# Kernel optimization log

Hardware: AMD Instinct MI355X
Metric: run time of the kernel (lower is better)

## Reference

```python
import jax, jax.numpy as jnp
import numpy as np

N_UP, N_DOWN, M, D, K, F, L, B = 16, 16, 4, 128, 64, 32, 3, 1024
N = N_UP + N_DOWN
H_W = 45  # round(sqrt(F*K)), hidden dim of the 2-layer w MLP
LOG2 = float(np.log(2.0))


def ssp(x):
    # shifted softplus activation used by deepqmc
    return jax.nn.softplus(x) - LOG2


def _pair_blocks(n_up, n_down):
    # replicate idx_perm(N,2) grouped by i, then idx_pair_spin partition
    n = n_up + n_down
    i = np.repeat(np.arange(n), n - 1)
    j = np.concatenate([np.concatenate([np.arange(k), np.arange(k + 1, n)]) for k in range(n)])
    blocks = []
    for mi, mj, ri, rj in [(True, True, n_up, max(n_up - 1, 0)),
                           (True, False, n_up, n_down),
                           (False, True, n_down, n_up),
                           (False, False, n_down, max(n_down - 1, 0))]:
        mask = ((i < n_up) == mi) & ((j < n_up) == mj)
        blocks.append((i[mask].reshape(ri, rj), j[mask].reshape(ri, rj)))
    return blocks

_BLOCKS = _pair_blocks(N_UP, N_DOWN)
_CHANS = [0, 1, 1, 0]  # same, anti, anti, same (w/g channel index; 2 = nuclear)


def setup_inputs() -> dict:
    key = jax.random.key(0)
    ks = jax.random.split(key, 12)
    s = 0.1
    return {
        'edges_elec': jax.random.normal(ks[0], (B, N, N, F), jnp.float32),
        'edges_nuc': jax.random.normal(ks[1], (B, N, M, F), jnp.float32),
        'X': jax.random.normal(ks[2], (1, D), jnp.float32) * s,
        'Y': jax.random.normal(ks[3], (M, K), jnp.float32) * s,
        'wW1': jax.random.normal(ks[4], (L, 3, H_W, F), jnp.float32) * s,
        'wb1': jax.random.normal(ks[5], (L, 3, H_W), jnp.float32) * s,
        'wW2': jax.random.normal(ks[6], (L, 3, K, H_W), jnp.float32) * s,
        'wb2': jax.random.normal(ks[7], (L, 3, K), jnp.float32) * s,
        'hW': jax.random.normal(ks[8], (L, K, D), jnp.float32) * s,
        'hb': jax.random.normal(ks[9], (L, K), jnp.float32) * s,
        'gW': jax.random.normal(ks[10], (L, 3, D, K), jnp.float32) * s,
        'gb': jax.random.normal(ks[11], (L, 3, D), jnp.float32) * s,
    }


def reference(edges_elec, edges_nuc, X, Y, wW1, wb1, wW2, wb2, hW, hb, gW, gb):
    def w_mlp(l, c, e):
        # 2-layer log-dim MLP: F -> H_W -> K with SSP in between
        return ssp(e @ wW1[l, c].T + wb1[l, c]) @ wW2[l, c].T + wb2[l, c]

    b = edges_nuc.shape[0]
    x = jnp.broadcast_to(X, (b, N, D))  # initial electron embeddings (n_up==n_down)
    for l in range(L):
        h = x @ hW[l].T + hb[l]  # shared h subnet: [b,N,K]
        zs = []
        for (ii, jj), c in zip(_BLOCKS, _CHANS):
            e = edges_elec[:, ii, jj, :]               # [b, ri, rj, F] gather
            msg = w_mlp(l, c, e) * h[:, jj, :]          # [b, ri, rj, K]
            zs.append(msg.sum(axis=-2))                 # segment-sum over j
        z_same = jnp.concatenate([zs[0], zs[3]], axis=-2)  # up then down
        z_anti = jnp.concatenate([zs[1], zs[2]], axis=-2)
        z_nuc = jnp.einsum('bnmk,mk->bnk', w_mlp(l, 2, edges_nuc), Y)
        update = (z_same @ gW[l, 0].T + gb[l, 0]
                  + z_anti @ gW[l, 1].T + gb[l, 1]
                  + z_nuc @ gW[l, 2].T + gb[l, 2])
        x = x + update  # resnet
    return x
```

## Files before the change

kernel.cpp:

```cpp
#include <hip/hip_runtime.h>
#include <math.h>

#define N_   32
#define NUP_ 16
#define M_   4
#define D_   128
#define K_   64
#define F_   32
#define H_   45
#define L_   3
#define LOG2_ 0.69314718055994530942f

typedef __attribute__((ext_vector_type(8))) short short8;
typedef __attribute__((ext_vector_type(4))) float float4v;

__device__ __forceinline__ float ssp(float v) {
    return __logf(fmaf(0.5f, __expf(v), 0.5f));
}

__device__ __forceinline__ unsigned short f2bf(float x) {
    unsigned int u = __float_as_uint(x);
    return (unsigned short)((u + 0x7FFFu + ((u >> 16) & 1u)) >> 16);
}

__device__ __forceinline__ unsigned int cvtpk(float x, float y) {
    unsigned int r;
    asm("v_cvt_pk_bf16_f32 %0, %1, %2" : "=v"(r) : "v"(x), "v"(y));
    return r;
}

__global__ __launch_bounds__(256) void prep_kernel(
    const float* __restrict__ wW1, const float* __restrict__ wb2_unused,
    const float* __restrict__ wW2, const float* __restrict__ wb2,
    const float* __restrict__ gW,  const float* __restrict__ hW,
    const float* __restrict__ gb,
    short* __restrict__ w1B, short* __restrict__ w2B,
    short* __restrict__ gB,  short* __restrict__ hB, float* __restrict__ gbs)
{
    int blk = blockIdx.x;
    int t = threadIdx.x;
    if (blk < 27) {
        int lc = blk / 3, nt = blk % 3;
        short* dst = w1B + (size_t)blk * 512;
        for (int idx = t; idx < 512; idx += 256) {
            int lane = idx >> 3, jj = idx & 7;
            int k = ((lane >> 4) << 3) + jj;
            int n = nt * 16 + (lane & 15);
            float v = (n < H_) ? wW1[((size_t)lc * H_ + n) * F_ + k] : 0.0f;
            dst[idx] = (short)f2bf(v);
        }
    } else if (blk < 99) {
        int b3 = blk - 27;
        int lc = b3 >> 3, rem = b3 & 7, ks = rem >> 2, nt = rem & 3;
        short* dst = w2B + (size_t)b3 * 512;
        for (int idx = t; idx < 512; idx += 256) {
            int lane = idx >> 3, jj = idx & 7;
            int p = ks * 32 + ((lane >> 4) << 3) + jj;
            int n = nt * 16 + (lane & 15);
            float v;
            if (p == 3) v = wb2[(size_t)lc * K_ + n];
            else if ((p & 3) < 3) {
                int u = (p & 3) * 16 + (p >> 2);
                v = (u < H_) ? wW2[((size_t)lc * K_ + n) * H_ + u] : 0.0f;
            } else v = 0.0f;
            dst[idx] = (short)f2bf(v);
        }
    } else if (blk < 243) {
        int g = blk - 99;
        int l = g / 48, rem = g % 48;
        short* dst = gB + (size_t)g * 512;
        for (int idx = t; idx < 512; idx += 256) {
            int lane = idx >> 3, jj = idx & 7;
            int k = (rem >> 3) * 32 + ((lane >> 4) << 3) + jj;
            int c = k >> 6, kk = k & 63;
            int n = ((rem & 7) * 16) + (lane & 15);
            dst[idx] = (short)f2bf(gW[(((size_t)l * 3 + c) * D_ + n) * K_ + kk]);
        }
    } else if (blk < 275) {
        int hh = blk - 243;
        int li = hh >> 4, rem = hh & 15;
        short* dst = hB + (size_t)hh * 512;
        for (int idx = t; idx < 512; idx += 256) {
            int lane = idx >> 3, jj = idx & 7;
            int p = (rem >> 2) * 32 + ((lane >> 4) << 3) + jj;
            int d = (p & 7) * 16 + (p >> 3);
            int n = ((rem & 3) * 16) + (lane & 15);
            dst[idx] = (short)f2bf(hW[(((size_t)(li + 1)) * K_ + n) * D_ + d]);
        }
    } else {
        for (int idx = t; idx < 384; idx += 256) {
            int l = idx >> 7, d = idx & 127;
            gbs[idx] = gb[((size_t)l * 3 + 0) * D_ + d]
                     + gb[((size_t)l * 3 + 1) * D_ + d]
                     + gb[((size_t)l * 3 + 2) * D_ + d];
        }
    }
}

__global__ __launch_bounds__(64) void h0_kernel(
    const float* __restrict__ X, const float* __restrict__ hW,
    const float* __restrict__ hb, float* __restrict__ h0)
{
    int k = threadIdx.x;
    float a = hb[k];
    const float* w = hW + (size_t)k * D_;
    #pragma unroll 8
    for (int dd = 0; dd < D_; ++dd) a += w[dd] * X[dd];
    h0[k] = a;
}

#define WSTRIDE 68
#define HDS 72
__global__ __launch_bounds__(256, 8) void edge_kernel(
    const float* __restrict__ ee, const float* __restrict__ en,
    const float* __restrict__ Y,
    const short* __restrict__ w1B, const float* __restrict__ wb1,
    const short* __restrict__ w2B,
    const float* __restrict__ h, const float* __restrict__ h0,
    unsigned short* __restrict__ zb, int l, int hmode)
{
    __shared__ float wrow[36 * WSTRIDE];
    __shared__ short hd_s[4][16 * HDS];

    const int tid  = threadIdx.x;
    const int wv   = tid >> 6;
    const int lane = tid & 63;
    const int quad = lane >> 4;
    const int l16  = lane & 15;
    const int b    = blockIdx.x >> 3;
    const int i    = ((blockIdx.x & 7) << 2) + wv;
    const int bi   = (b << 5) + i;

    {
        int row = tid >> 3;
        int col = (tid & 7) * 8;
        const float* src = hmode ? (h + ((size_t)(b * N_ + row)) * K_ + col) : (h0 + col);
        float4 v0 = *(const float4*)(src);
        float4 v1 = *(const float4*)(src + 4);
        *(float4*)(wrow + row * WSTRIDE + col)     = v0;
        *(float4*)(wrow + row * WSTRIDE + col + 4) = v1;
        if (tid < 32) {
            int r2 = tid >> 3, o2 = (tid & 7) * 8;
            float4 y0 = *(const float4*)(Y + (size_t)r2 * K_ + o2);
            float4 y1 = *(const float4*)(Y + (size_t)r2 * K_ + o2 + 4);
            *(float4*)(wrow + (32 + r2) * WSTRIDE + o2)     = y0;
            *(float4*)(wrow + (32 + r2) * WSTRIDE + o2 + 4) = y1;
        }
    }
    __syncthreads();

    const int cA = (i < NUP_) ? 0 : 1;
    short* hd = hd_s[wv];
    const float c3  = (l16 == 0) ? 1.0f : 0.0f;
    const int   ri  = i & 3;
    const int   tqi = (i & 15) >> 2;
    const int   tti = i >> 4;

    #pragma unroll
    for (int t = 0; t < 3; ++t) {
        const int c  = (t == 2) ? 2 : ((t == 0) ? cA : 1 - cA);
        const int lc = l * 3 + c;

        float4 fa = {0.f, 0.f, 0.f, 0.f}, fb = {0.f, 0.f, 0.f, 0.f};
        if (t < 2) {
            const float* ep = ee + (((size_t)bi * N_) + t * 16 + l16) * F_ + quad * 8;
            fa = *(const float4*)(ep);
            fb = *(const float4*)(ep + 4);
        } else if (l16 < M_) {
            const float* np = en + (((size_t)bi * M_) + l16) * F_ + quad * 8;
            fa = *(const float4*)(np);
            fb = *(const float4*)(np + 4);
        }
        union { short8 s; unsigned int u[4]; } A;
        A.u[0] = cvtpk(fa.x, fa.y); A.u[1] = cvtpk(fa.z, fa.w);
        A.u[2] = cvtpk(fb.x, fb.y); A.u[3] = cvtpk(fb.z, fb.w);

        float4v acc1[3];
        #pragma unroll
        for (int nt = 0; nt < 3; ++nt) {
            int col = nt * 16 + l16;
            float b1c = (col < H_) ? wb1[(size_t)lc * H_ + col] : 0.0f;
            acc1[nt] = (float4v){b1c, b1c, b1c, b1c};
            short8 bf = *(const short8*)(w1B + (((size_t)lc * 3 + nt) << 9) + (lane << 3));
            acc1[nt] = __builtin_amdgcn_mfma_f32_16x16x32_bf16(A.s, bf, acc1[nt], 0, 0, 0);
        }

        const bool deadq = (t < 2) ? ((tti == t) && (quad == tqi)) : (quad != 0);
        #pragma unroll
        for (int r = 0; r < 4; ++r) {
            float s0 = ssp(acc1[0][r]);
            float s1 = ssp(acc1[1][r]);
            float s2 = ssp(acc1[2][r]);
            uint2 pr;
            pr.x = cvtpk(s0, s1);
            pr.y = cvtpk(s2, c3);
            const bool dead = deadq && ((t == 2) || (r == ri));
            if (dead) { pr.x = 0u; pr.y = 0u; }
            *(uint2*)(hd + (quad * 4 + r) * HDS + 4 * l16) = pr;
        }

        float4v acc2[4];
        #pragma unroll
        for (int nt = 0; nt < 4; ++nt) acc2[nt] = (float4v){0.f, 0.f, 0.f, 0.f};
        #pragma unroll
        for (int ks = 0; ks < 2; ++ks) {
            short8 a2 = *(const short8*)(hd + l16 * HDS + ks * 32 + quad * 8);
            #pragma unroll
            for (int nt = 0; nt < 4; ++nt) {
                short8 bf = *(const short8*)(w2B + ((((size_t)lc * 2 + ks) * 4 + nt) << 9) + (lane << 3));
                acc2[nt] = __builtin_amdgcn_mfma_f32_16x16x32_bf16(a2, bf, acc2[nt], 0, 0, 0);
            }
        }

        float p0 = 0.f, p1 = 0.f, p2 = 0.f, p3 = 0.f;
        #pragma unroll
        for (int r = 0; r < 4; ++r) {
            const int jrow = (t == 2) ? (32 + r) : (t * 16 + quad * 4 + r);
            const float* wr = wrow + jrow * WSTRIDE + l16;
            p0 += acc2[0][r] * wr[0];
            p1 += acc2[1][r] * wr[16];
            p2 += acc2[2][r] * wr[32];
            p3 += acc2[3][r] * wr[48];
        }

        const bool qlo = (quad & 1) != 0;
        const bool qhi = (quad & 2) != 0;
        float u  = qlo ? p1 : p0;
        float us = qlo ? p0 : p1;
        u += __shfl_xor(u * 0.0f + us, 16);
        float w  = qlo ? p3 : p2;
        float ws = qlo ? p2 : p3;
        w += __shfl_xor(ws, 16);
        float v  = qhi ? w : u;
        float vs = qhi ? u : w;
        v += __shfl_xor(vs, 32);

        unsigned int pk = cvtpk(v, v);
        zb[(size_t)bi * 192 + c * 64 + lane] = (unsigned short)pk;
    }
}

#define HXS 136
__global__ __launch_bounds__(256) void fuse_kernel(
    const unsigned short* __restrict__ zb, const short* __restrict__ gB,
    const float* __restrict__ gbs, const float* __restrict__ X,
    const short* __restrict__ hB, const float* __restrict__ hb,
    float* __restrict__ xout, float* __restrict__ hout,
    int l, int first, int compute_h)
{
    __shared__ short hx_s[4][16 * HXS];

    const int tid  = threadIdx.x;
    const int wv   = tid >> 6;
    const int lane = tid & 63;
    const int quad = lane >> 4;
    const int l16  = lane & 15;
    const int bi0  = (blockIdx.x * 4 + wv) * 16;

    float4v ax[8];
    #pragma unroll
    for (int nt = 0; nt < 8; ++nt) ax[nt] = (float4v){0.f, 0.f, 0.f, 0.f};
    const short* gb_ = gB + (size_t)l * 48 * 512;
    const short* zrow = (const short*)zb + ((size_t)(bi0 + l16)) * 192;
    #pragma unroll
    for (int ks = 0; ks < 6; ++ks) {
        short8 az = *(const short8*)(zrow + ks * 32 + quad * 8);
        #pragma unroll
        for (int nt = 0; nt < 8; ++nt) {
            short8 bf = *(const short8*)(gb_ + (((size_t)ks * 8 + nt) << 9) + (lane << 3));
            ax[nt] = __builtin_amdgcn_mfma_f32_16x16x32_bf16(az, bf, ax[nt], 0, 0, 0);
        }
    }

    float gv[8], xb[8];
    #pragma unroll
    for (int nt = 0; nt < 8; ++nt) {
        gv[nt] = gbs[(size_t)l * D_ + nt * 16 + l16];
        if (first) xb[nt] = X[nt * 16 + l16];
    }
    short* hx = hx_s[wv];
    #pragma unroll
    for (int r = 0; r < 4; ++r) {
        int row = quad * 4 + r;
        size_t gi = ((size_t)(bi0 + row)) * D_ + l16;
        float xv[8];
        #pragma unroll
        for (int nt = 0; nt < 8; ++nt) {
            float xo = (first ? xb[nt] : xout[gi + nt * 16]) + gv[nt] + ax[nt][r];
            xout[gi + nt * 16] = xo;
            xv[nt] = xo;
        }
        if (compute_h) {
            union { short8 s; unsigned int u[4]; } P;
            P.u[0] = cvtpk(xv[0], xv[1]); P.u[1] = cvtpk(xv[2], xv[3]);
            P.u[2] = cvtpk(xv[4], xv[5]); P.u[3] = cvtpk(xv[6], xv[7]);
            *(short8*)(hx + row * HXS + 8 * l16) = P.s;
        }
    }
    if (!compute_h) return;

    float4v ah[4];
    #pragma unroll
    for (int nt = 0; nt < 4; ++nt) ah[nt] = (float4v){0.f, 0.f, 0.f, 0.f};
    const short* hb_ = hB + (size_t)l * 16 * 512;
    #pragma unroll
    for (int ks = 0; ks < 4; ++ks) {
        short8 a = *(const short8*)(hx + l16 * HXS + ks * 32 + quad * 8);
        #pragma unroll
        for (int nt = 0; nt < 4; ++nt) {
            short8 bf = *(const short8*)(hb_ + (((size_t)ks * 4 + nt) << 9) + (lane << 3));
            ah[nt] = __builtin_amdgcn_mfma_f32_16x16x32_bf16(a, bf, ah[nt], 0, 0, 0);
        }
    }
    float hbv[4];
    #pragma unroll
    for (int nt = 0; nt < 4; ++nt) hbv[nt] = hb[((size_t)(l + 1)) * K_ + nt * 16 + l16];
    #pragma unroll
    for (int nt = 0; nt < 4; ++nt)
        #pragma unroll
        for (int r = 0; r < 4; ++r)
            hout[((size_t)(bi0 + quad * 4 + r)) * K_ + nt * 16 + l16] = ah[nt][r] + hbv[nt];
}

extern "C" void kernel_launch(void* const* d_in, const int* in_sizes, int n_in,
                              void* d_out, int out_size, void* d_ws, size_t ws_size,
                              hipStream_t stream)
{
    const float* ee  = (const float*)d_in[0];
    const float* en  = (const float*)d_in[1];
    const float* X   = (const float*)d_in[2];
    const float* Y   = (const float*)d_in[3];
    const float* wW1 = (const float*)d_in[4];
    const float* wb1 = (const float*)d_in[5];
    const float* wW2 = (const float*)d_in[6];
    const float* wb2 = (const float*)d_in[7];
    const float* hW  = (const float*)d_in[8];
    const float* hb  = (const float*)d_in[9];
    const float* gW  = (const float*)d_in[10];
    const float* gb  = (const float*)d_in[11];
    float* xout = (float*)d_out;

    char* ws = (char*)d_ws;
    float*          h   = (float*)(ws);
    unsigned short* zb  = (unsigned short*)(ws + 8388608);
    float*          h0  = (float*)(ws + 8388608 + 12582912);
    short*          w1B = (short*)(ws + 20971520 + 256);
    short*          w2B = w1B + (size_t)27 * 512;
    short*          gB  = w2B + (size_t)72 * 512;
    short*          hB  = gB  + (size_t)144 * 512;
    float*          gbs = (float*)(hB + (size_t)32 * 512);

    prep_kernel<<<276, 256, 0, stream>>>(wW1, wb1, wW2, wb2, gW, hW, gb,
                                         w1B, w2B, gB, hB, gbs);
    h0_kernel<<<1, 64, 0, stream>>>(X, hW, hb, h0);

    edge_kernel<<<8192, 256, 0, stream>>>(ee, en, Y, w1B, wb1, w2B, h, h0, zb, 0, 0);
    fuse_kernel<<<512, 256, 0, stream>>>(zb, gB, gbs, X, hB, hb, xout, h, 0, 1, 1);
    edge_kernel<<<8192, 256, 0, stream>>>(ee, en, Y, w1B, wb1, w2B, h, h0, zb, 1, 1);
    fuse_kernel<<<512, 256, 0, stream>>>(zb, gB, gbs, X, hB, hb, xout, h, 1, 0, 1);
    edge_kernel<<<8192, 256, 0, stream>>>(ee, en, Y, w1B, wb1, w2B, h, h0, zb, 2, 1);
    fuse_kernel<<<512, 256, 0, stream>>>(zb, gB, gbs, X, hB, hb, xout, h, 2, 0, 0);
}
```

Baseline: 441.2 us.

## Compute nuclear channel once per block and split fuse kernel across wave pairs

```diff
diff --git a/kernel.cpp b/kernel.cpp
--- a/kernel.cpp
+++ b/kernel.cpp
@@ -157,20 +157,13 @@
     const int   tti = i >> 4;
 
     #pragma unroll
-    for (int t = 0; t < 3; ++t) {
-        const int c  = (t == 2) ? 2 : ((t == 0) ? cA : 1 - cA);
+    for (int t = 0; t < 2; ++t) {
+        const int c  = (t == 0) ? cA : 1 - cA;
         const int lc = l * 3 + c;
 
-        float4 fa = {0.f, 0.f, 0.f, 0.f}, fb = {0.f, 0.f, 0.f, 0.f};
-        if (t < 2) {
-            const float* ep = ee + (((size_t)bi * N_) + t * 16 + l16) * F_ + quad * 8;
-            fa = *(const float4*)(ep);
-            fb = *(const float4*)(ep + 4);
-        } else if (l16 < M_) {
-            const float* np = en + (((size_t)bi * M_) + l16) * F_ + quad * 8;
-            fa = *(const float4*)(np);
-            fb = *(const float4*)(np + 4);
-        }
+        const float* ep = ee + (((size_t)bi * N_) + t * 16 + l16) * F_ + quad * 8;
+        float4 fa = *(const float4*)(ep);
+        float4 fb = *(const float4*)(ep + 4);
         union { short8 s; unsigned int u[4]; } A;
         A.u[0] = cvtpk(fa.x, fa.y); A.u[1] = cvtpk(fa.z, fa.w);
         A.u[2] = cvtpk(fb.x, fb.y); A.u[3] = cvtpk(fb.z, fb.w);
@@ -185,7 +178,7 @@
             acc1[nt] = __builtin_amdgcn_mfma_f32_16x16x32_bf16(A.s, bf, acc1[nt], 0, 0, 0);
         }
 
-        const bool deadq = (t < 2) ? ((tti == t) && (quad == tqi)) : (quad != 0);
+        const bool deadq = (tti == t) && (quad == tqi);
         #pragma unroll
         for (int r = 0; r < 4; ++r) {
             float s0 = ssp(acc1[0][r]);
@@ -194,8 +187,7 @@
             uint2 pr;
             pr.x = cvtpk(s0, s1);
             pr.y = cvtpk(s2, c3);
-            const bool dead = deadq && ((t == 2) || (r == ri));
-            if (dead) { pr.x = 0u; pr.y = 0u; }
+            if (deadq && (r == ri)) { pr.x = 0u; pr.y = 0u; }
             *(uint2*)(hd + (quad * 4 + r) * HDS + 4 * l16) = pr;
         }
 
@@ -215,7 +207,7 @@
         float p0 = 0.f, p1 = 0.f, p2 = 0.f, p3 = 0.f;
         #pragma unroll
         for (int r = 0; r < 4; ++r) {
-            const int jrow = (t == 2) ? (32 + r) : (t * 16 + quad * 4 + r);
+            const int jrow = t * 16 + quad * 4 + r;
             const float* wr = wrow + jrow * WSTRIDE + l16;
             p0 += acc2[0][r] * wr[0];
             p1 += acc2[1][r] * wr[16];
@@ -227,7 +219,7 @@
         const bool qhi = (quad & 2) != 0;
         float u  = qlo ? p1 : p0;
         float us = qlo ? p0 : p1;
-        u += __shfl_xor(u * 0.0f + us, 16);
+        u += __shfl_xor(us, 16);
         float w  = qlo ? p3 : p2;
         float ws = qlo ? p2 : p3;
         w += __shfl_xor(ws, 16);
@@ -235,8 +227,67 @@
         float vs = qhi ? u : w;
         v += __shfl_xor(vs, 32);
 
-        unsigned int pk = cvtpk(v, v);
-        zb[(size_t)bi * 192 + c * 64 + lane] = (unsigned short)pk;
+        zb[(size_t)bi * 192 + c * 64 + lane] = (unsigned short)cvtpk(v, v);
+    }
+
+    if (wv == 0) {
+        const int lc = l * 3 + 2;
+
+        const float* np = en + ((size_t)bi * M_ + l16) * F_ + quad * 8;
+        float4 fa = *(const float4*)(np);
+        float4 fb = *(const float4*)(np + 4);
+        union { short8 s; unsigned int u[4]; } A;
+        A.u[0] = cvtpk(fa.x, fa.y); A.u[1] = cvtpk(fa.z, fa.w);
+        A.u[2] = cvtpk(fb.x, fb.y); A.u[3] = cvtpk(fb.z, fb.w);
+
+        float4v acc1[3];
+        #pragma unroll
+        for (int nt = 0; nt < 3; ++nt) {
+            int col = nt * 16 + l16;
+            float b1c = (col < H_) ? wb1[(size_t)lc * H_ + col] : 0.0f;
+            acc1[nt] = (float4v){b1c, b1c, b1c, b1c};
+            short8 bf = *(const short8*)(w1B + (((size_t)lc * 3 + nt) << 9) + (lane << 3));
+            acc1[nt] = __builtin_amdgcn_mfma_f32_16x16x32_bf16(A.s, bf, acc1[nt], 0, 0, 0);
+        }
+
+        #pragma unroll
+        for (int r = 0; r < 4; ++r) {
+            float s0 = ssp(acc1[0][r]);
+            float s1 = ssp(acc1[1][r]);
+            float s2 = ssp(acc1[2][r]);
+            uint2 pr;
+            pr.x = cvtpk(s0, s1);
+            pr.y = cvtpk(s2, c3);
+            *(uint2*)(hd + (quad * 4 + r) * HDS + 4 * l16) = pr;
+        }
+
+        float4v acc2[4];
+        #pragma unroll
+        for (int nt = 0; nt < 4; ++nt) acc2[nt] = (float4v){0.f, 0.f, 0.f, 0.f};
+        #pragma unroll
+        for (int ks = 0; ks < 2; ++ks) {
+            short8 a2 = *(const short8*)(hd + l16 * HDS + ks * 32 + quad * 8);
+            #pragma unroll
+            for (int nt = 0; nt < 4; ++nt) {
+                short8 bf = *(const short8*)(w2B + ((((size_t)lc * 2 + ks) * 4 + nt) << 9) + (lane << 3));
+                acc2[nt] = __builtin_amdgcn_mfma_f32_16x16x32_bf16(a2, bf, acc2[nt], 0, 0, 0);
+            }
+        }
+
+        float p0 = 0.f, p1 = 0.f, p2 = 0.f, p3 = 0.f;
+        #pragma unroll
+        for (int r = 0; r < 4; ++r) {
+            const float* wr = wrow + (32 + r) * WSTRIDE + l16;
+            p0 += acc2[0][r] * wr[0];
+            p1 += acc2[1][r] * wr[16];
+            p2 += acc2[2][r] * wr[32];
+            p3 += acc2[3][r] * wr[48];
+        }
+        unsigned short* zo = zb + (size_t)(bi + quad) * 192 + 128 + l16;
+        zo[0]  = (unsigned short)cvtpk(p0, p0);
+        zo[16] = (unsigned short)cvtpk(p1, p1);
+        zo[32] = (unsigned short)cvtpk(p2, p2);
+        zo[48] = (unsigned short)cvtpk(p3, p3);
     }
 }
 
@@ -248,78 +299,82 @@
     float* __restrict__ xout, float* __restrict__ hout,
     int l, int first, int compute_h)
 {
-    __shared__ short hx_s[4][16 * HXS];
+    __shared__ short hx_s[2][16 * HXS];
 
     const int tid  = threadIdx.x;
     const int wv   = tid >> 6;
     const int lane = tid & 63;
     const int quad = lane >> 4;
     const int l16  = lane & 15;
-    const int bi0  = (blockIdx.x * 4 + wv) * 16;
-
-    float4v ax[8];
-    #pragma unroll
-    for (int nt = 0; nt < 8; ++nt) ax[nt] = (float4v){0.f, 0.f, 0.f, 0.f};
+    const int pair = wv >> 1;
+    const int half = wv & 1;
+    const int nt0  = half * 4;
+    const int bi0  = (blockIdx.x * 2 + pair) * 16;
+
+    float4v ax[4];
+    #pragma unroll
+    for (int nt = 0; nt < 4; ++nt) ax[nt] = (float4v){0.f, 0.f, 0.f, 0.f};
     const short* gb_ = gB + (size_t)l * 48 * 512;
     const short* zrow = (const short*)zb + ((size_t)(bi0 + l16)) * 192;
     #pragma unroll
     for (int ks = 0; ks < 6; ++ks) {
         short8 az = *(const short8*)(zrow + ks * 32 + quad * 8);
         #pragma unroll
-        for (int nt = 0; nt < 8; ++nt) {
-            short8 bf = *(const short8*)(gb_ + (((size_t)ks * 8 + nt) << 9) + (lane << 3));
+        for (int nt = 0; nt < 4; ++nt) {
+            short8 bf = *(const short8*)(gb_ + (((size_t)ks * 8 + nt0 + nt) << 9) + (lane << 3));
             ax[nt] = __builtin_amdgcn_mfma_f32_16x16x32_bf16(az, bf, ax[nt], 0, 0, 0);
         }
     }
 
-    float gv[8], xb[8];
-    #pragma unroll
-    for (int nt = 0; nt < 8; ++nt) {
-        gv[nt] = gbs[(size_t)l * D_ + nt * 16 + l16];
-        if (first) xb[nt] = X[nt * 16 + l16];
-    }
-    short* hx = hx_s[wv];
+    float gv[4], xb[4];
+    #pragma unroll
+    for (int nt = 0; nt < 4; ++nt) {
+        gv[nt] = gbs[(size_t)l * D_ + (nt0 + nt) * 16 + l16];
+        if (first) xb[nt] = X[(nt0 + nt) * 16 + l16];
+    }
+    short* hx = hx_s[pair];
     #pragma unroll
     for (int r = 0; r < 4; ++r) {
         int row = quad * 4 + r;
         size_t gi = ((size_t)(bi0 + row)) * D_ + l16;
-        float xv[8];
-        #pragma unroll
-        for (int nt = 0; nt < 8; ++nt) {
-            float xo = (first ? xb[nt] : xout[gi + nt * 16]) + gv[nt] + ax[nt][r];
-            xout[gi + nt * 16] = xo;
+        float xv[4];
+        #pragma unroll
+        for (int nt = 0; nt < 4; ++nt) {
+            float xo = (first ? xb[nt] : xout[gi + (nt0 + nt) * 16]) + gv[nt] + ax[nt][r];
+            xout[gi + (nt0 + nt) * 16] = xo;
             xv[nt] = xo;
         }
         if (compute_h) {
-            union { short8 s; unsigned int u[4]; } P;
-            P.u[0] = cvtpk(xv[0], xv[1]); P.u[1] = cvtpk(xv[2], xv[3]);
-            P.u[2] = cvtpk(xv[4], xv[5]); P.u[3] = cvtpk(xv[6], xv[7]);
-            *(short8*)(hx + row * HXS + 8 * l16) = P.s;
+            uint2 P;
+            P.x = cvtpk(xv[0], xv[1]);
+            P.y = cvtpk(xv[2], xv[3]);
+            *(uint2*)(hx + row * HXS + 8 * l16 + 4 * half) = P;
         }
     }
     if (!compute_h) return;
-
-    float4v ah[4];
-    #pragma unroll
-    for (int nt = 0; nt < 4; ++nt) ah[nt] = (float4v){0.f, 0.f, 0.f, 0.f};
+    __syncthreads();
+
+    float4v ah[2];
+    #pragma unroll
+    for (int nt = 0; nt < 2; ++nt) ah[nt] = (float4v){0.f, 0.f, 0.f, 0.f};
     const short* hb_ = hB + (size_t)l * 16 * 512;
     #pragma unroll
     for (int ks = 0; ks < 4; ++ks) {
         short8 a = *(const short8*)(hx + l16 * HXS + ks * 32 + quad * 8);
         #pragma unroll
-        for (int nt = 0; nt < 4; ++nt) {
-            short8 bf = *(const short8*)(hb_ + (((size_t)ks * 4 + nt) << 9) + (lane << 3));
+        for (int nt = 0; nt < 2; ++nt) {
+            short8 bf = *(const short8*)(hb_ + (((size_t)ks * 4 + half * 2 + nt) << 9) + (lane << 3));
             ah[nt] = __builtin_amdgcn_mfma_f32_16x16x32_bf16(a, bf, ah[nt], 0, 0, 0);
         }
     }
-    float hbv[4];
-    #pragma unroll
-    for (int nt = 0; nt < 4; ++nt) hbv[nt] = hb[((size_t)(l + 1)) * K_ + nt * 16 + l16];
-    #pragma unroll
-    for (int nt = 0; nt < 4; ++nt)
+    float hbv[2];
+    #pragma unroll
+    for (int nt = 0; nt < 2; ++nt) hbv[nt] = hb[((size_t)(l + 1)) * K_ + (half * 2 + nt) * 16 + l16];
+    #pragma unroll
+    for (int nt = 0; nt < 2; ++nt)
         #pragma unroll
         for (int r = 0; r < 4; ++r)
-            hout[((size_t)(bi0 + quad * 4 + r)) * K_ + nt * 16 + l16] = ah[nt][r] + hbv[nt];
+            hout[((size_t)(bi0 + quad * 4 + r)) * K_ + (half * 2 + nt) * 16 + l16] = ah[nt][r] + hbv[nt];
 }
 
 extern "C" void kernel_launch(void* const* d_in, const int* in_sizes, int n_in,
@@ -355,9 +410,9 @@
     h0_kernel<<<1, 64, 0, stream>>>(X, hW, hb, h0);
 
     edge_kernel<<<8192, 256, 0, stream>>>(ee, en, Y, w1B, wb1, w2B, h, h0, zb, 0, 0);
-    fuse_kernel<<<512, 256, 0, stream>>>(zb, gB, gbs, X, hB, hb, xout, h, 0, 1, 1);
+    fuse_kernel<<<1024, 256, 0, stream>>>(zb, gB, gbs, X, hB, hb, xout, h, 0, 1, 1);
     edge_kernel<<<8192, 256, 0, stream>>>(ee, en, Y, w1B, wb1, w2B, h, h0, zb, 1, 1);
-    fuse_kernel<<<512, 256, 0, stream>>>(zb, gB, gbs, X, hB, hb, xout, h, 1, 0, 1);
+    fuse_kernel<<<1024, 256, 0, stream>>>(zb, gB, gbs, X, hB, hb, xout, h, 1, 0, 1);
     edge_kernel<<<8192, 256, 0, stream>>>(ee, en, Y, w1B, wb1, w2B, h, h0, zb, 2, 1);
-    fuse_kernel<<<512, 256, 0, stream>>>(zb, gB, gbs, X, hB, hb, xout, h, 2, 0, 0);
-}
+    fuse_kernel<<<1024, 256, 0, stream>>>(zb, gB, gbs, X, hB, hb, xout, h, 2, 0, 0);
+}
```

Measured after the change: 400.4 us. -9.2%, faster.
